# Kernel tuning notes

Hardware: AMD Instinct MI355X
Metric: run time of the kernel (lower is better)

## Reference

```python
import jax, jax.numpy as jnp
import numpy as np
import math

# static config (mirrors Model.__init__)
NUM_SEGMENTS = 4
TILE = 32
NUM_SEQS = 8
Q_LEN = 128           # query tokens per sequence (uniform)
SEQ_LEN = 2048        # total seq len (context + query)
NUM_Q_HEADS = 32
NUM_KV_HEADS = 8
HEAD_SIZE = 128       # == head_size_padded (required for the torch code to type-check)
BLK_SIZE = 16
MAX_BLOCKS = SEQ_LEN // BLK_SIZE
NUM_BLKS = NUM_SEQS * MAX_BLOCKS


def setup_inputs() -> dict:
    key = jax.random.key(0)
    k1, k2, k3, k4 = jax.random.split(key, 4)
    num_tokens = NUM_SEQS * Q_LEN
    query = jax.random.normal(k1, (num_tokens, NUM_Q_HEADS, HEAD_SIZE), jnp.float32)
    # torch indexes key_cache[pb, kv, :, off, 0] -> 5D with trailing singleton
    key_cache = jax.random.normal(k2, (NUM_BLKS, NUM_KV_HEADS, HEAD_SIZE, BLK_SIZE, 1), jnp.float32)
    value_cache = jax.random.normal(k3, (NUM_BLKS, NUM_KV_HEADS, HEAD_SIZE, BLK_SIZE), jnp.float32)
    # scattered (permuted) physical block assignment, vLLM-style
    block_tables = jax.random.permutation(k4, NUM_BLKS).reshape(NUM_SEQS, MAX_BLOCKS).astype(jnp.int32)
    seq_lens = jnp.full((NUM_SEQS,), SEQ_LEN, dtype=jnp.int32)
    query_start_len = jnp.arange(NUM_SEQS + 1, dtype=jnp.int32) * Q_LEN
    return {
        "query": query,
        "key_cache": key_cache,
        "value_cache": value_cache,
        "block_tables": block_tables,
        "seq_lens": seq_lens,
        "query_start_len": query_start_len,
        "scale": 1.0 / math.sqrt(HEAD_SIZE),
        "k_scale": 1.0,
        "v_scale": 1.0,
        "softcap": 30.0,
    }


def _paged_segmented_attention(query, key_cache, value_cache, block_tables, seq_lens, scale, softcap):
    S, M = block_tables.shape
    T, H, D = query.shape
    Hkv = key_cache.shape[1]
    G = H // Hkv                  # queries per kv head (GQA)
    B = key_cache.shape[3]
    Q = T // S                    # uniform query length per sequence
    L = M * B                     # KV length covered by the block table
    # block-table gather of paged KV -> [S, Hkv, L, D]
    k_all = key_cache[block_tables][..., 0]                              # [S, M, Hkv, D, B]
    k_all = jnp.transpose(k_all, (0, 2, 1, 4, 3)).reshape(S, Hkv, L, D)
    v_all = jnp.transpose(value_cache[block_tables], (0, 2, 1, 4, 3)).reshape(S, Hkv, L, D)
    q = query.reshape(S, Q, Hkv, G, D).astype(jnp.float32)
    scores = scale * jnp.einsum('sqhgd,shld->shgql', q, k_all.astype(jnp.float32))  # [S,Hkv,G,Q,L]
    if softcap > 0:
        scores = softcap * jnp.tanh(scores / softcap)
    ctx = seq_lens - Q                                                   # context length per seq [S]
    qabs = ctx[:, None] + jnp.arange(Q)[None, :]                         # absolute q positions [S,Q]
    kpos = jnp.arange(L)
    causal = kpos[None, None, :] <= qabs[:, :, None]                     # [S,Q,L]
    # keys per segment = tiles_per_segment * 32, per sequence
    span = (-(-seq_lens // (NUM_SEGMENTS * TILE))) * TILE                # [S]
    neg_inf = jnp.float32(-jnp.inf)
    v32 = v_all.astype(jnp.float32)
    outs = []
    for seg in range(NUM_SEGMENTS):                                      # small fixed loop
        seg_mask = (kpos[None, :] >= seg * span[:, None]) & (kpos[None, :] < (seg + 1) * span[:, None])  # [S,L]
        mask = (causal & seg_mask[:, None, :])[:, None, None, :, :]      # [S,1,1,Q,L]
        masked = jnp.where(mask, scores, neg_inf)
        m = masked.max(axis=-1)
        m_safe = jnp.where(m > neg_inf, m, 0.0)                          # torch's zero-clamp of -inf max
        p = jnp.exp(masked - m_safe[..., None])                          # [S,Hkv,G,Q,L]
        # NOTE: torch returns the UNNORMALIZED accumulator (expsum is discarded)
        acc = jnp.einsum('shgql,shld->shgqd', p, v32)
        outs.append(acc)
    out = jnp.stack(outs, axis=-2)                                       # [S,Hkv,G,Q,NSEG,D]
    out = jnp.transpose(out, (0, 3, 1, 2, 4, 5)).reshape(T, H, NUM_SEGMENTS, D)
    return out.astype(query.dtype)


def reference(query, key_cache, value_cache, block_tables, seq_lens, query_start_len, scale, k_scale, v_scale, softcap):
    # fp32 cache path: k_scale/v_scale dequantization is a no-op (torch applies it only for fp8 caches).
    # query_start_len is consistent with uniform Q_LEN per sequence (used implicitly via reshape).
    return _paged_segmented_attention(query, key_cache, value_cache, block_tables, seq_lens,
                                      float(scale), float(softcap))
```

## Files before the change

### kernel.cpp

```cpp
#include <hip/hip_runtime.h>

#define NSEQ   8
#define QLEN   128
#define NQH    32
#define NKVH   8
#define GQ     4
#define HD     128
#define BLK    16
#define MAXBLK 128
#define LTOT   2048
#define NSEGC  4
#define TILEC  32

typedef __attribute__((ext_vector_type(8)))  short  shortx8;
typedef __attribute__((ext_vector_type(4)))  short  shortx4;
typedef __attribute__((ext_vector_type(16))) float  floatx16;
typedef __attribute__((ext_vector_type(4)))  float  fx4;

__device__ __forceinline__ short f2bf(float f) {
    unsigned u = __float_as_uint(f);
    u = (u + 0x7FFFu + ((u >> 16) & 1u)) >> 16;
    return (short)(unsigned short)u;
}

__global__ __launch_bounds__(512, 2) void psa_kernel(
    const float* __restrict__ query,
    const float* __restrict__ key_cache,
    const float* __restrict__ value_cache,
    const int*   __restrict__ block_tables,
    const int*   __restrict__ seq_lens,
    const float* __restrict__ scale_p,
    const float* __restrict__ softcap_p,
    float* __restrict__ out)
{
    __shared__ __align__(16) short kbuf[2][16][64][8];
    __shared__ __align__(16) short vbuf[2][8][128][8];
    __shared__ __align__(16) short pbuf[8][8][32][8];

    const int bi   = blockIdx.x;
    const int p_lo = bi & 7;
    const int qh   = (bi >> 3) & 1;
    const int pp   = (bi >> 4) * 8 + p_lo;
    const int seg  = pp & 3;
    const int h    = (pp >> 2) & 7;
    const int s    = pp >> 5;

    const int tid  = threadIdx.x;
    const int w    = tid >> 6;
    const int lane = tid & 63;
    const int lo   = lane & 31;
    const int hi   = lane >> 5;

    const float NEG_INF = -__builtin_inff();
    const float scale   = *scale_p;
    const float softcap = *softcap_p;
    const int   seq     = seq_lens[s];
    const int   ctx     = seq - QLEN;
    const int   span    = ((seq + NSEGC * TILEC - 1) / (NSEGC * TILEC)) * TILEC;
    const int   seg_start = seg * span;
    int seg_len = LTOT - seg_start;
    if (seg_len > span) seg_len = span;
    const int NT = (seg_len > 0) ? ((seg_len + 63) >> 6) : 0;

    const float LOG2E = 1.4426950408889634f;
    const bool  do_cap = (softcap > 0.0f);
    const float c1 = do_cap ? (2.0f * LOG2E / softcap) : 0.0f;
    const float c2 = do_cap ? (softcap * LOG2E) : 0.0f;

    const int r_base = qh * 256 + w * 32;
    const int qb     = r_base & 127;
    const int g      = r_base >> 7;
    const int qrow   = qb + lo;
    const int q_off  = ((s * QLEN + qrow) * NQH + h * GQ + g) * HD;
    shortx8 qfrag[8];
#pragma unroll
    for (int ks = 0; ks < 8; ++ks) {
        const float* qp = query + q_off + ks * 16 + hi * 8;
        fx4 a = *(const fx4*)qp;
        fx4 b = *(const fx4*)(qp + 4);
        shortx8 v8;
        v8[0] = f2bf(a[0] * scale); v8[1] = f2bf(a[1] * scale);
        v8[2] = f2bf(a[2] * scale); v8[3] = f2bf(a[3] * scale);
        v8[4] = f2bf(b[0] * scale); v8[5] = f2bf(b[1] * scale);
        v8[6] = f2bf(b[2] * scale); v8[7] = f2bf(b[3] * scale);
        qfrag[ks] = v8;
    }

    const int bt_base = s * MAXBLK;

    float kreg[2][8];
    fx4   vreg[2][2];
    const int kb  = tid & 63;
    const int kdc = tid >> 6;
    const int vd  = tid & 127;
    const int vlh = tid >> 7;

    auto stage_load = [&](int nt) {
        {
            int l_glob = seg_start + nt * 64 + kb;
            if (l_glob >= LTOT) l_glob = LTOT - 1;
            const int pb = block_tables[bt_base + (l_glob >> 4)];
            const float* kp = key_cache + (pb * NKVH + h) * (HD * BLK) + (l_glob & 15);
#pragma unroll
            for (int ic = 0; ic < 2; ++ic)
#pragma unroll
                for (int j = 0; j < 8; ++j)
                    kreg[ic][j] = kp[((kdc + ic * 8) * 8 + j) * BLK];
        }
        {
#pragma unroll
            for (int ic = 0; ic < 2; ++ic) {
                const int lslab = vlh + ic * 4;
                int l_glob = seg_start + nt * 64 + lslab * 8;
                if (l_glob >= LTOT) l_glob = LTOT - 8;
                const int pb = block_tables[bt_base + (l_glob >> 4)];
                const float* vp = value_cache + ((pb * NKVH + h) * HD + vd) * BLK + (l_glob & 15);
                vreg[ic][0] = *(const fx4*)vp;
                vreg[ic][1] = *(const fx4*)(vp + 4);
            }
        }
    };
    auto stage_write = [&](int bb) {
#pragma unroll
        for (int ic = 0; ic < 2; ++ic) {
            shortx8 v8;
#pragma unroll
            for (int j = 0; j < 8; ++j) v8[j] = f2bf(kreg[ic][j]);
            *(shortx8*)(&kbuf[bb][kdc + ic * 8][kb][0]) = v8;
        }
#pragma unroll
        for (int ic = 0; ic < 2; ++ic) {
            shortx8 v8;
#pragma unroll
            for (int j = 0; j < 4; ++j) {
                v8[j]     = f2bf(vreg[ic][0][j]);
                v8[4 + j] = f2bf(vreg[ic][1][j]);
            }
            *(shortx8*)(&vbuf[bb][vlh + ic * 4][vd][0]) = v8;
        }
    };

    floatx16 acc[4];
#pragma unroll
    for (int dt = 0; dt < 4; ++dt)
#pragma unroll
        for (int i = 0; i < 16; ++i) acc[dt][i] = 0.0f;
    float m_run = NEG_INF;

    if (NT > 0) { stage_load(0); stage_write(0); }

    for (int nt = 0; nt < NT; ++nt) {
        const int bb = nt & 1;
        __syncthreads();
        const bool pre = (nt + 1 < NT);
        if (pre) stage_load(nt + 1);

        const int tile_l0 = seg_start + nt * 64;
        const bool need_mask = (tile_l0 + 63 > ctx + qb) || (nt * 64 + 63 >= seg_len);

#pragma unroll
        for (int nsub = 0; nsub < 2; ++nsub) {
            floatx16 c;
#pragma unroll
            for (int i = 0; i < 16; ++i) c[i] = 0.0f;
#pragma unroll
            for (int ks = 0; ks < 8; ++ks) {
                shortx8 af = *(const shortx8*)(&kbuf[bb][ks * 2 + hi][nsub * 32 + lo][0]);
                c = __builtin_amdgcn_mfma_f32_32x32x16_bf16(af, qfrag[ks], c, 0, 0, 0);
            }
            float z[16];
            float mloc = NEG_INF;
#pragma unroll
            for (int r = 0; r < 16; ++r) {
                const float si = c[r];
                float zz;
                if (do_cap) {
                    const float u  = __builtin_amdgcn_exp2f(si * c1);
                    const float rr = __builtin_amdgcn_rcpf(u + 1.0f);
                    zz = c2 - (2.0f * c2) * rr;
                } else {
                    zz = si * LOG2E;
                }
                if (need_mask) {
                    const int key   = nsub * 32 + (r & 3) + 8 * (r >> 2) + 4 * hi;
                    const int l_loc = nt * 64 + key;
                    const bool ok = (l_loc < seg_len) && (tile_l0 + key <= ctx + qb + lo);
                    zz = ok ? zz : NEG_INF;
                }
                z[r] = zz;
                mloc = fmaxf(mloc, zz);
            }
            mloc  = fmaxf(mloc, __shfl_xor(mloc, 32, 64));
            m_run = fmaxf(m_run, mloc);
#pragma unroll
            for (int rq = 0; rq < 4; ++rq) {
                shortx4 pk;
#pragma unroll
                for (int i = 0; i < 4; ++i)
                    pk[i] = f2bf(__builtin_amdgcn_exp2f(z[rq * 4 + i]));
                *(shortx4*)(&pbuf[w][nsub * 4 + rq][lo][hi * 4]) = pk;
            }
        }

#pragma unroll
        for (int ks = 0; ks < 4; ++ks) {
            shortx8 pf = *(const shortx8*)(&pbuf[w][ks * 2 + hi][lo][0]);
#pragma unroll
            for (int dt = 0; dt < 4; ++dt) {
                shortx8 vf = *(const shortx8*)(&vbuf[bb][ks * 2 + hi][dt * 32 + lo][0]);
                acc[dt] = __builtin_amdgcn_mfma_f32_32x32x16_bf16(pf, vf, acc[dt], 0, 0, 0);
            }
        }

        if (pre) stage_write(bb ^ 1);
    }

    const float scv = (m_run == NEG_INF) ? 0.0f : __builtin_amdgcn_exp2f(-m_run);
    const int out_base = ((s * QLEN + qb) * NQH + (h * GQ + g)) * (NSEGC * HD) + seg * HD + lo;
#pragma unroll
    for (int r = 0; r < 16; ++r) {
        const int row = (r & 3) + 8 * (r >> 2) + 4 * hi;
        const float sc = __shfl(scv, row, 64);
        const int ob = out_base + row * (NQH * NSEGC * HD);
#pragma unroll
        for (int dt = 0; dt < 4; ++dt)
            out[ob + dt * 32] = acc[dt][r] * sc;
    }
}

extern "C" void kernel_launch(void* const* d_in, const int* in_sizes, int n_in,
                              void* d_out, int out_size, void* d_ws, size_t ws_size,
                              hipStream_t stream) {
    const float* query        = (const float*)d_in[0];
    const float* key_cache    = (const float*)d_in[1];
    const float* value_cache  = (const float*)d_in[2];
    const int*   block_tables = (const int*)d_in[3];
    const int*   seq_lens     = (const int*)d_in[4];
    const float* scale_p      = (const float*)d_in[6];
    const float* softcap_p    = (const float*)d_in[9];

    psa_kernel<<<dim3(512), dim3(512), 0, stream>>>(
        query, key_cache, value_cache, block_tables, seq_lens,
        scale_p, softcap_p, (float*)d_out);
}
```

Measured before the change: 238.1 us.

## Keep P in registers via permlane32 swap and use hardware bf16 conversion

Drops the per-wave LDS round-trip for the softmax probabilities P. The bf16-packed P fragments are rearranged across wave halves with permlane32_swap and fed straight into the PV MFMA, one 32-key subtile at a time. All float-to-bf16 conversions now use the native __bf16 cast with packed pairs instead of manual integer rounding. This removes 32 KB of shared memory and the LDS store/load traffic for P, but depends on the permlane lane mapping exactly matching the MFMA operand layout.

```diff
diff --git a/kernel.cpp b/kernel.cpp
--- a/kernel.cpp
+++ b/kernel.cpp
@@ -13,14 +13,17 @@
 #define TILEC  32
 
 typedef __attribute__((ext_vector_type(8)))  short  shortx8;
-typedef __attribute__((ext_vector_type(4)))  short  shortx4;
 typedef __attribute__((ext_vector_type(16))) float  floatx16;
 typedef __attribute__((ext_vector_type(4)))  float  fx4;
+typedef __attribute__((ext_vector_type(4)))  int    intx4;
+typedef __attribute__((ext_vector_type(2)))  __bf16 bf16x2;
 
 __device__ __forceinline__ short f2bf(float f) {
-    unsigned u = __float_as_uint(f);
-    u = (u + 0x7FFFu + ((u >> 16) & 1u)) >> 16;
-    return (short)(unsigned short)u;
+    return __builtin_bit_cast(short, (__bf16)f);
+}
+__device__ __forceinline__ int pk2(float a, float b) {
+    bf16x2 t; t[0] = (__bf16)a; t[1] = (__bf16)b;
+    return __builtin_bit_cast(int, t);
 }
 
 __global__ __launch_bounds__(512, 2) void psa_kernel(
@@ -35,7 +38,6 @@
 {
     __shared__ __align__(16) short kbuf[2][16][64][8];
     __shared__ __align__(16) short vbuf[2][8][128][8];
-    __shared__ __align__(16) short pbuf[8][8][32][8];
 
     const int bi   = blockIdx.x;
     const int p_lo = bi & 7;
@@ -78,12 +80,9 @@
         const float* qp = query + q_off + ks * 16 + hi * 8;
         fx4 a = *(const fx4*)qp;
         fx4 b = *(const fx4*)(qp + 4);
-        shortx8 v8;
-        v8[0] = f2bf(a[0] * scale); v8[1] = f2bf(a[1] * scale);
-        v8[2] = f2bf(a[2] * scale); v8[3] = f2bf(a[3] * scale);
-        v8[4] = f2bf(b[0] * scale); v8[5] = f2bf(b[1] * scale);
-        v8[6] = f2bf(b[2] * scale); v8[7] = f2bf(b[3] * scale);
-        qfrag[ks] = v8;
+        intx4 w4 = { pk2(a[0] * scale, a[1] * scale), pk2(a[2] * scale, a[3] * scale),
+                     pk2(b[0] * scale, b[1] * scale), pk2(b[2] * scale, b[3] * scale) };
+        qfrag[ks] = __builtin_bit_cast(shortx8, w4);
     }
 
     const int bt_base = s * MAXBLK;
@@ -120,23 +119,18 @@
             }
         }
     };
-    auto stage_write = [&](int bb) {
+    auto stage_write = [&](int bb_) {
 #pragma unroll
         for (int ic = 0; ic < 2; ++ic) {
-            shortx8 v8;
-#pragma unroll
-            for (int j = 0; j < 8; ++j) v8[j] = f2bf(kreg[ic][j]);
-            *(shortx8*)(&kbuf[bb][kdc + ic * 8][kb][0]) = v8;
+            intx4 w4 = { pk2(kreg[ic][0], kreg[ic][1]), pk2(kreg[ic][2], kreg[ic][3]),
+                         pk2(kreg[ic][4], kreg[ic][5]), pk2(kreg[ic][6], kreg[ic][7]) };
+            *(intx4*)(&kbuf[bb_][kdc + ic * 8][kb][0]) = w4;
         }
 #pragma unroll
         for (int ic = 0; ic < 2; ++ic) {
-            shortx8 v8;
-#pragma unroll
-            for (int j = 0; j < 4; ++j) {
-                v8[j]     = f2bf(vreg[ic][0][j]);
-                v8[4 + j] = f2bf(vreg[ic][1][j]);
-            }
-            *(shortx8*)(&vbuf[bb][vlh + ic * 4][vd][0]) = v8;
+            intx4 w4 = { pk2(vreg[ic][0][0], vreg[ic][0][1]), pk2(vreg[ic][0][2], vreg[ic][0][3]),
+                         pk2(vreg[ic][1][0], vreg[ic][1][1]), pk2(vreg[ic][1][2], vreg[ic][1][3]) };
+            *(intx4*)(&vbuf[bb_][vlh + ic * 4][vd][0]) = w4;
         }
     };
 
@@ -192,23 +186,29 @@
             }
             mloc  = fmaxf(mloc, __shfl_xor(mloc, 32, 64));
             m_run = fmaxf(m_run, mloc);
-#pragma unroll
-            for (int rq = 0; rq < 4; ++rq) {
-                shortx4 pk;
-#pragma unroll
-                for (int i = 0; i < 4; ++i)
-                    pk[i] = f2bf(__builtin_amdgcn_exp2f(z[rq * 4 + i]));
-                *(shortx4*)(&pbuf[w][nsub * 4 + rq][lo][hi * 4]) = pk;
-            }
-        }
-
-#pragma unroll
-        for (int ks = 0; ks < 4; ++ks) {
-            shortx8 pf = *(const shortx8*)(&pbuf[w][ks * 2 + hi][lo][0]);
-#pragma unroll
-            for (int dt = 0; dt < 4; ++dt) {
-                shortx8 vf = *(const shortx8*)(&vbuf[bb][ks * 2 + hi][dt * 32 + lo][0]);
-                acc[dt] = __builtin_amdgcn_mfma_f32_32x32x16_bf16(pf, vf, acc[dt], 0, 0, 0);
+
+            int A[8];
+#pragma unroll
+            for (int i = 0; i < 8; ++i)
+                A[i] = pk2(__builtin_amdgcn_exp2f(z[2 * i]),
+                           __builtin_amdgcn_exp2f(z[2 * i + 1]));
+            auto s0 = __builtin_amdgcn_permlane32_swap(A[0], A[2], false, false);
+            auto s1 = __builtin_amdgcn_permlane32_swap(A[1], A[3], false, false);
+            auto s2 = __builtin_amdgcn_permlane32_swap(A[4], A[6], false, false);
+            auto s3 = __builtin_amdgcn_permlane32_swap(A[5], A[7], false, false);
+            intx4 w0 = { (int)s0[0], (int)s1[0], (int)s0[1], (int)s1[1] };
+            intx4 w1 = { (int)s2[0], (int)s3[0], (int)s2[1], (int)s3[1] };
+            shortx8 pf[2] = { __builtin_bit_cast(shortx8, w0),
+                              __builtin_bit_cast(shortx8, w1) };
+
+#pragma unroll
+            for (int ks2 = 0; ks2 < 2; ++ks2) {
+                const int slab = (nsub * 2 + ks2) * 2 + hi;
+#pragma unroll
+                for (int dt = 0; dt < 4; ++dt) {
+                    shortx8 vf = *(const shortx8*)(&vbuf[bb][slab][dt * 32 + lo][0]);
+                    acc[dt] = __builtin_amdgcn_mfma_f32_32x32x16_bf16(pf[ks2], vf, acc[dt], 0, 0, 0);
+                }
             }
         }
 
```

New measurement: 231.2 us. 2.9% less time.
